# Optimization experiments

Hardware: AMD Instinct MI355X
Metric: run time of the kernel (lower is better)

## Reference

```python
import jax, jax.numpy as jnp
import numpy as np


def _maxpool2x2(x):
    # x: [B, C, H, W] -> [B, C, H//2, W//2]
    B, C, H, W = x.shape
    return x.reshape(B, C, H // 2, 2, W // 2, 2).max(axis=(3, 5))


def setup_inputs() -> dict:
    key = jax.random.key(0)
    ks = jax.random.split(key, 6)
    B, C, H, W = 16, 64, 64, 64
    x = jax.random.normal(ks[0], (B, C, H, W), dtype=jnp.float32)
    w_theta = jax.random.normal(ks[1], (C // 8, C), dtype=jnp.float32) * (1.0 / np.sqrt(C))
    w_phi = jax.random.normal(ks[2], (C // 8, C), dtype=jnp.float32) * (1.0 / np.sqrt(C))
    w_g = jax.random.normal(ks[3], (C // 2, C), dtype=jnp.float32) * (1.0 / np.sqrt(C))
    w_o = jax.random.normal(ks[4], (C, C // 2), dtype=jnp.float32) * (1.0 / np.sqrt(C // 2))
    gamma = jax.random.normal(ks[5], (), dtype=jnp.float32)
    return {"x": x, "w_theta": w_theta, "w_phi": w_phi, "w_g": w_g, "w_o": w_o, "gamma": gamma}


def reference(x, w_theta, w_phi, w_g, w_o, gamma):
    B, C, H, W = x.shape
    S = H * W  # full spatial size
    # 1x1 convs == channel matmuls
    theta = jnp.einsum('oc,bchw->bohw', w_theta, x)            # [B, C/8, H, W]
    phi = _maxpool2x2(jnp.einsum('oc,bchw->bohw', w_phi, x))   # [B, C/8, H/2, W/2]
    g = _maxpool2x2(jnp.einsum('oc,bchw->bohw', w_g, x))       # [B, C/2, H/2, W/2]
    theta_f = theta.reshape(B, C // 8, S)                      # [B, C/8, S]
    phi_f = phi.reshape(B, C // 8, S // 4)                     # [B, C/8, S/4]
    g_f = g.reshape(B, C // 2, S // 4)                         # [B, C/2, S/4]
    # beta = softmax(theta^T @ phi) over key dim
    scores = jnp.einsum('bcs,bct->bst', theta_f, phi_f)        # [B, S, S/4]
    beta = jax.nn.softmax(scores, axis=-1)
    attn = jnp.einsum('bct,bst->bcs', g_f, beta)               # [B, C/2, S]
    o = jnp.einsum('oc,bcs->bos', w_o, attn).reshape(B, C, H, W)
    return gamma * o + x
```

## Files before the change

### kernel.cpp

```cpp
#include <hip/hip_runtime.h>

#define B 16
#define C 64
#define SS 4096
#define TT 1024
#define CQ 8
#define CG 32

typedef _Float16 h4 __attribute__((ext_vector_type(4)));
typedef float f32x16 __attribute__((ext_vector_type(16)));

#if __has_builtin(__builtin_amdgcn_exp2f)
#define EXP2(x) __builtin_amdgcn_exp2f(x)
#else
#define EXP2(x) exp2f(x)
#endif

#define MFMA328(a, b, c) __builtin_amdgcn_mfma_f32_32x32x8f16((a), (b), (c), 0, 0, 0)

__global__ __launch_bounds__(256) void k_proj(
        const float* __restrict__ x, const float* __restrict__ w_theta,
        const float* __restrict__ w_phi, const float* __restrict__ w_g,
        _Float16* __restrict__ theta_t, _Float16* __restrict__ phi_t,
        _Float16* __restrict__ g_blk) {
    int tid = threadIdx.x;
    int W = blockIdx.x * 4 + (tid >> 6);
    int l = tid & 63;
    int ln = l & 31, hi = l >> 5;
    int b = W >> 6, ws = W & 63;
    int rp = ws >> 1, wt = ws & 1;
    int sA = rp * 128 + wt * 32 + ln;

    const float LOG2E = 1.44269504088896f;
    float wsc = 1.f;
    const float* wr0;
    if (ln < 8)       { wr0 = w_theta + ln * C; wsc = LOG2E; }
    else if (ln < 16) { wr0 = w_phi + (ln - 8) * C; }
    else              { wr0 = w_g + (ln - 16) * C; }
    const float* wr1 = w_g + (16 + (ln & 15)) * C;
    bool t1v = ln < 16;

    h4 wa0[8], wa1[8];
#pragma unroll
    for (int kk = 0; kk < 8; ++kk) {
        float4 v0 = *(const float4*)&wr0[8 * kk + 4 * hi];
        float4 v1 = *(const float4*)&wr1[8 * kk + 4 * hi];
        wa0[kk][0] = (_Float16)(v0.x * wsc);
        wa0[kk][1] = (_Float16)(v0.y * wsc);
        wa0[kk][2] = (_Float16)(v0.z * wsc);
        wa0[kk][3] = (_Float16)(v0.w * wsc);
        wa1[kk][0] = t1v ? (_Float16)v1.x : (_Float16)0.f;
        wa1[kk][1] = t1v ? (_Float16)v1.y : (_Float16)0.f;
        wa1[kk][2] = t1v ? (_Float16)v1.z : (_Float16)0.f;
        wa1[kk][3] = t1v ? (_Float16)v1.w : (_Float16)0.f;
    }

    const float* xb = x + ((size_t)b << 18);
    float xA[8][4], xB[8][4];
#pragma unroll
    for (int kk = 0; kk < 8; ++kk)
#pragma unroll
        for (int i = 0; i < 4; ++i) {
            int c = 8 * kk + 4 * hi + i;
            xA[kk][i] = xb[((size_t)c << 12) + sA];
            xB[kk][i] = xb[((size_t)c << 12) + sA + 64];
        }

    f32x16 aA0, aA1, aB0, aB1;
#pragma unroll
    for (int r = 0; r < 16; ++r) { aA0[r] = 0.f; aA1[r] = 0.f; aB0[r] = 0.f; aB1[r] = 0.f; }

#pragma unroll
    for (int kk = 0; kk < 8; ++kk) {
        h4 bA, bB;
#pragma unroll
        for (int i = 0; i < 4; ++i) {
            bA[i] = (_Float16)xA[kk][i];
            bB[i] = (_Float16)xB[kk][i];
        }
        aA0 = MFMA328(wa0[kk], bA, aA0);
        aB0 = MFMA328(wa0[kk], bB, aB0);
        aA1 = MFMA328(wa1[kk], bA, aA1);
        aB1 = MFMA328(wa1[kk], bB, aB1);
    }

    {
        h4 tv;
#pragma unroll
        for (int r = 0; r < 4; ++r) tv[r] = (_Float16)aA0[r];
        *(h4*)&theta_t[(size_t)((b << 12) + sA) * 8 + 4 * hi] = tv;
#pragma unroll
        for (int r = 0; r < 4; ++r) tv[r] = (_Float16)aB0[r];
        *(h4*)&theta_t[(size_t)((b << 12) + sA + 64) * 8 + 4 * hi] = tv;
    }

    int t = rp * 32 + wt * 16 + (ln >> 1);
    float pv[4];
#pragma unroll
    for (int j = 0; j < 4; ++j) {
        float m = fmaxf(aA0[4 + j], aB0[4 + j]);
        m = fmaxf(m, __shfl_xor(m, 1));
        pv[j] = m;
    }
    float gv[4][4];
#pragma unroll
    for (int j = 0; j < 4; ++j) {
        float m0 = fmaxf(aA0[8 + j],  aB0[8 + j]);
        float m1 = fmaxf(aA0[12 + j], aB0[12 + j]);
        float m2 = fmaxf(aA1[j],      aB1[j]);
        float m3 = fmaxf(aA1[4 + j],  aB1[4 + j]);
        gv[0][j] = fmaxf(m0, __shfl_xor(m0, 1));
        gv[1][j] = fmaxf(m1, __shfl_xor(m1, 1));
        gv[2][j] = fmaxf(m2, __shfl_xor(m2, 1));
        gv[3][j] = fmaxf(m3, __shfl_xor(m3, 1));
    }
    if ((l & 1) == 0) {
        h4 pj;
#pragma unroll
        for (int j = 0; j < 4; ++j) pj[j] = (_Float16)pv[j];
        *(h4*)&phi_t[(size_t)((b << 10) + t) * 8 + 4 * hi] = pj;
        _Float16* gb = g_blk + ((size_t)(b * 256 + (t >> 2)) * 32) * 4 + (t & 3);
#pragma unroll
        for (int part = 0; part < 4; ++part) {
            int cbase = part * 8 + 4 * hi;
#pragma unroll
            for (int j = 0; j < 4; ++j)
                gb[(size_t)(cbase + j) * 4] = (_Float16)gv[part][j];
        }
    }
}

__global__ __launch_bounds__(512, 4) void k_attn(
        const float* __restrict__ x, const _Float16* __restrict__ theta_t,
        const _Float16* __restrict__ phi_t, const _Float16* __restrict__ g_blk,
        const float* __restrict__ w_o, const float* __restrict__ gamma_p,
        float* __restrict__ out) {
    __shared__ __align__(16) char smem[81920];
    _Float16* g_sh   = (_Float16*)smem;
    _Float16* phi_sh = (_Float16*)(smem + 65536);
    float (*accx)[16][64] = (float (*)[16][64])smem;
    float (*mlx)[2][64]   = (float (*)[2][64])(smem + 32768);

    int tid = threadIdx.x;
    int bid = blockIdx.x;
    int wg = (bid & 7) * 64 + (bid >> 3);
    int b = wg >> 5;
    int s0 = (wg & 31) * 128;
    int w = tid >> 6;
    int l = tid & 63;
    int ln = l & 31, hi = l >> 5;
    int sub = w & 3, half = w >> 2;
    int sw = s0 + sub * 32;
    int h16 = half * 16;

    {
        const float4* srcg = (const float4*)(g_blk + (size_t)b * (256 * 128));
        float4* dstg = (float4*)smem;
#pragma unroll
        for (int i = 0; i < 8; ++i)
            dstg[tid + 512 * i] = srcg[tid + 512 * i];
        const float4* srcp = (const float4*)(phi_t + ((size_t)b << 10) * 8);
        float4* dstp = (float4*)phi_sh;
#pragma unroll
        for (int i = 0; i < 2; ++i)
            dstp[tid + 512 * i] = srcp[tid + 512 * i];
    }

    h4 bth = *(const h4*)&theta_t[(size_t)((b << 12) + sw + ln) * 8 + 4 * hi];

    const _Float16* phib = phi_t + ((size_t)b << 10) * 8;

    f32x16 zero;
#pragma unroll
    for (int r = 0; r < 16; ++r) zero[r] = 0.f;

#define LD_PHI(t_) (*(const h4*)&phib[(size_t)((t_) * 32 + ln) * 8 + 4 * hi])
#define LD_PHI_S(t_) (*(const h4*)&phi_sh[(size_t)((t_) * 32 + ln) * 8 + 4 * hi])
#define LD_G_S(dst, t_)                                                        \
    {                                                                          \
        _Pragma("unroll")                                                      \
        for (int kk = 0; kk < 4; ++kk)                                         \
            dst[kk] = *(const h4*)&g_sh[(size_t)(((t_) * 8 + 2 * kk + hi) * 32 + ln) * 4]; \
    }
#define FMAX16(dst, sc_)                                                       \
    {                                                                          \
        float y0 = fmaxf(sc_[0], sc_[1]),   y1 = fmaxf(sc_[2], sc_[3]);        \
        float y2 = fmaxf(sc_[4], sc_[5]),   y3 = fmaxf(sc_[6], sc_[7]);        \
        float y4 = fmaxf(sc_[8], sc_[9]),   y5 = fmaxf(sc_[10], sc_[11]);      \
        float y6 = fmaxf(sc_[12], sc_[13]), y7 = fmaxf(sc_[14], sc_[15]);      \
        y0 = fmaxf(y0, y1); y2 = fmaxf(y2, y3);                                \
        y4 = fmaxf(y4, y5); y6 = fmaxf(y6, y7);                                \
        y0 = fmaxf(y0, y2); y4 = fmaxf(y4, y6);                                \
        dst = fmaxf(dst, fmaxf(y0, y4));                                       \
    }

    float mx = -1e30f;
    {
        h4 pa = LD_PHI(h16);
        h4 pb = LD_PHI(h16 + 1);
#pragma unroll 2
        for (int tc = 0; tc < 16; tc += 2) {
            h4 pan = LD_PHI(h16 + ((tc + 2) & 15));
            h4 pbn = LD_PHI(h16 + ((tc + 3) & 15));
            f32x16 sa = MFMA328(pa, bth, zero);
            f32x16 sb = MFMA328(pb, bth, zero);
            FMAX16(mx, sa);
            FMAX16(mx, sb);
            pa = pan;
            pb = pbn;
        }
        mx = fmaxf(mx, __shfl_xor(mx, 32));
    }

    f32x16 cneg;
#pragma unroll
    for (int r = 0; r < 16; ++r) cneg[r] = -mx;

    __syncthreads();

    f32x16 accE = zero, accO = zero;
    float lsum = 0.f;

#pragma unroll 2
    for (int tc = 0; tc < 16; ++tc) {
        int t_ = h16 + tc;
        h4 ap = LD_PHI_S(t_);
        h4 ag[4];
        LD_G_S(ag, t_);

        f32x16 sc = MFMA328(ap, bth, cneg);

        h4 bp[4];
        float pa0 = 0.f, pa1 = 0.f;
#pragma unroll
        for (int kk = 0; kk < 4; ++kk)
#pragma unroll
            for (int i = 0; i < 4; ++i) {
                float p = EXP2(sc[4 * kk + i]);
                if (kk < 2) pa0 += p; else pa1 += p;
                bp[kk][i] = (_Float16)p;
            }
        lsum += pa0 + pa1;

        accE = MFMA328(ag[0], bp[0], accE);
        accO = MFMA328(ag[1], bp[1], accO);
        accE = MFMA328(ag[2], bp[2], accE);
        accO = MFMA328(ag[3], bp[3], accO);
    }
    f32x16 acc = accE + accO;
    lsum += __shfl_xor(lsum, 32);

    __syncthreads();

#pragma unroll
    for (int r = 0; r < 16; ++r) accx[w][r][l] = acc[r];
    mlx[w][0][l] = mx;
    mlx[w][1][l] = lsum;
    __syncthreads();

    int p = w ^ 4;
    float m2 = mlx[p][0][l], l2 = mlx[p][1][l];
    float M = fmaxf(mx, m2);
    float f1 = EXP2(mx - M), f2 = EXP2(m2 - M);
    float lt = lsum * f1 + l2 * f2;
    float linv = 1.f / lt;

    h4 bat[4];
#pragma unroll
    for (int kk = 0; kk < 4; ++kk)
#pragma unroll
        for (int i = 0; i < 4; ++i) {
            float a2 = accx[p][4 * kk + i][l];
            bat[kk][i] = (_Float16)((acc[4 * kk + i] * f1 + a2 * f2) * linv);
        }

    float gm = gamma_p[0];
    h4 a3[4];
#pragma unroll
    for (int kk = 0; kk < 4; ++kk) {
        float4 wv = *(const float4*)&w_o[(half * 32 + ln) * CG + 8 * kk + 4 * hi];
        a3[kk][0] = (_Float16)(wv.x * gm);
        a3[kk][1] = (_Float16)(wv.y * gm);
        a3[kk][2] = (_Float16)(wv.z * gm);
        a3[kk][3] = (_Float16)(wv.w * gm);
    }
    f32x16 d = MFMA328(a3[0], bat[0], zero);
    d = MFMA328(a3[1], bat[1], d);
    d = MFMA328(a3[2], bat[2], d);
    d = MFMA328(a3[3], bat[3], d);
#pragma unroll
    for (int r = 0; r < 16; ++r) {
        int ch = half * 32 + (r & 3) + 8 * (r >> 2) + 4 * hi;
        size_t idx = (((size_t)(b * C + ch)) << 12) + sw + ln;
        out[idx] = d[r] + x[idx];
    }
#undef LD_PHI
#undef LD_PHI_S
#undef LD_G_S
#undef FMAX16
}

extern "C" void kernel_launch(void* const* d_in, const int* in_sizes, int n_in,
                              void* d_out, int out_size, void* d_ws, size_t ws_size,
                              hipStream_t stream) {
    const float* x       = (const float*)d_in[0];
    const float* w_theta = (const float*)d_in[1];
    const float* w_phi   = (const float*)d_in[2];
    const float* w_g     = (const float*)d_in[3];
    const float* w_o     = (const float*)d_in[4];
    const float* gamma   = (const float*)d_in[5];
    float* out = (float*)d_out;

    _Float16* ws      = (_Float16*)d_ws;
    _Float16* theta_t = ws;
    _Float16* phi_t   = theta_t + (size_t)B * SS * 8;
    _Float16* g_blk   = phi_t + (size_t)B * TT * 8;

    k_proj<<<256, 256, 0, stream>>>(x, w_theta, w_phi, w_g, theta_t, phi_t, g_blk);
    k_attn<<<512, 512, 0, stream>>>(x, theta_t, phi_t, g_blk, w_o, gamma, out);
}
```

Before: 31.12 us.

## Switch attention kernel to 16x16x16 MFMA with 1024-thread blocks of 16-query waves

Rewrites k_attn to use 16x16x16 f16 MFMA tiles instead of 32x32x8. Each wave now handles 16 queries, and the block grows to 16 waves (1024 threads) so it still covers 128 queries, split into two halves over keys. Because K=16 is padded from 8 theta channels, half the lanes feed zero theta (kg>=2), which wastes part of the score MFMA. The exp/softmax work per MFMA is smaller and there are more waves per block, aiming at better latency hiding. The risk is larger register and shared-memory contention at 1024 threads, and score-MFMA efficiency is halved.

```diff
diff --git a/kernel.cpp b/kernel.cpp
--- a/kernel.cpp
+++ b/kernel.cpp
@@ -8,6 +8,7 @@
 #define CG 32
 
 typedef _Float16 h4 __attribute__((ext_vector_type(4)));
+typedef float f32x4 __attribute__((ext_vector_type(4)));
 typedef float f32x16 __attribute__((ext_vector_type(16)));
 
 #if __has_builtin(__builtin_amdgcn_exp2f)
@@ -17,6 +18,7 @@
 #endif
 
 #define MFMA328(a, b, c) __builtin_amdgcn_mfma_f32_32x32x8f16((a), (b), (c), 0, 0, 0)
+#define MFMA16(a, b, c) __builtin_amdgcn_mfma_f32_16x16x16f16((a), (b), (c), 0, 0, 0)
 
 __global__ __launch_bounds__(256) void k_proj(
         const float* __restrict__ x, const float* __restrict__ w_theta,
@@ -130,7 +132,7 @@
     }
 }
 
-__global__ __launch_bounds__(512, 4) void k_attn(
+__global__ __launch_bounds__(1024, 8) void k_attn(
         const float* __restrict__ x, const _Float16* __restrict__ theta_t,
         const _Float16* __restrict__ phi_t, const _Float16* __restrict__ g_blk,
         const float* __restrict__ w_o, const float* __restrict__ gamma_p,
@@ -138,8 +140,8 @@
     __shared__ __align__(16) char smem[81920];
     _Float16* g_sh   = (_Float16*)smem;
     _Float16* phi_sh = (_Float16*)(smem + 65536);
-    float (*accx)[16][64] = (float (*)[16][64])smem;
-    float (*mlx)[2][64]   = (float (*)[2][64])(smem + 32768);
+    float (*accx)[8][64] = (float (*)[8][64])smem;
+    float (*mlx)[2][64]  = (float (*)[2][64])(smem + 32768);
 
     int tid = threadIdx.x;
     int bid = blockIdx.x;
@@ -148,156 +150,123 @@
     int s0 = (wg & 31) * 128;
     int w = tid >> 6;
     int l = tid & 63;
-    int ln = l & 31, hi = l >> 5;
-    int sub = w & 3, half = w >> 2;
-    int sw = s0 + sub * 32;
-    int h16 = half * 16;
+    int ln4 = l & 15, kg = l >> 4;
+    int ssub = w & 7, half = w >> 3;
+    int sw = s0 + ssub * 16;
+    int hc = half * 32;
+    int off = (kg & 1) * 4;
 
     {
         const float4* srcg = (const float4*)(g_blk + (size_t)b * (256 * 128));
         float4* dstg = (float4*)smem;
 #pragma unroll
-        for (int i = 0; i < 8; ++i)
-            dstg[tid + 512 * i] = srcg[tid + 512 * i];
+        for (int i = 0; i < 4; ++i)
+            dstg[tid + 1024 * i] = srcg[tid + 1024 * i];
         const float4* srcp = (const float4*)(phi_t + ((size_t)b << 10) * 8);
-        float4* dstp = (float4*)phi_sh;
-#pragma unroll
-        for (int i = 0; i < 2; ++i)
-            dstp[tid + 512 * i] = srcp[tid + 512 * i];
-    }
-
-    h4 bth = *(const h4*)&theta_t[(size_t)((b << 12) + sw + ln) * 8 + 4 * hi];
+        ((float4*)phi_sh)[tid] = srcp[tid];
+    }
+
+    h4 bth = {};
+    if (kg < 2)
+        bth = *(const h4*)&theta_t[(size_t)((b << 12) + sw + ln4) * 8 + 4 * kg];
 
     const _Float16* phib = phi_t + ((size_t)b << 10) * 8;
-
-    f32x16 zero;
-#pragma unroll
-    for (int r = 0; r < 16; ++r) zero[r] = 0.f;
-
-#define LD_PHI(t_) (*(const h4*)&phib[(size_t)((t_) * 32 + ln) * 8 + 4 * hi])
-#define LD_PHI_S(t_) (*(const h4*)&phi_sh[(size_t)((t_) * 32 + ln) * 8 + 4 * hi])
-#define LD_G_S(dst, t_)                                                        \
-    {                                                                          \
-        _Pragma("unroll")                                                      \
-        for (int kk = 0; kk < 4; ++kk)                                         \
-            dst[kk] = *(const h4*)&g_sh[(size_t)(((t_) * 8 + 2 * kk + hi) * 32 + ln) * 4]; \
-    }
-#define FMAX16(dst, sc_)                                                       \
-    {                                                                          \
-        float y0 = fmaxf(sc_[0], sc_[1]),   y1 = fmaxf(sc_[2], sc_[3]);        \
-        float y2 = fmaxf(sc_[4], sc_[5]),   y3 = fmaxf(sc_[6], sc_[7]);        \
-        float y4 = fmaxf(sc_[8], sc_[9]),   y5 = fmaxf(sc_[10], sc_[11]);      \
-        float y6 = fmaxf(sc_[12], sc_[13]), y7 = fmaxf(sc_[14], sc_[15]);      \
-        y0 = fmaxf(y0, y1); y2 = fmaxf(y2, y3);                                \
-        y4 = fmaxf(y4, y5); y6 = fmaxf(y6, y7);                                \
-        y0 = fmaxf(y0, y2); y4 = fmaxf(y4, y6);                                \
-        dst = fmaxf(dst, fmaxf(y0, y4));                                       \
-    }
+    f32x4 zero4 = {0.f, 0.f, 0.f, 0.f};
 
     float mx = -1e30f;
     {
-        h4 pa = LD_PHI(h16);
-        h4 pb = LD_PHI(h16 + 1);
+        h4 pa = *(const h4*)&phib[(size_t)((hc + 0) * 16 + ln4) * 8 + off];
+        h4 pb = *(const h4*)&phib[(size_t)((hc + 1) * 16 + ln4) * 8 + off];
 #pragma unroll 2
-        for (int tc = 0; tc < 16; tc += 2) {
-            h4 pan = LD_PHI(h16 + ((tc + 2) & 15));
-            h4 pbn = LD_PHI(h16 + ((tc + 3) & 15));
-            f32x16 sa = MFMA328(pa, bth, zero);
-            f32x16 sb = MFMA328(pb, bth, zero);
-            FMAX16(mx, sa);
-            FMAX16(mx, sb);
+        for (int tc = 0; tc < 32; tc += 2) {
+            h4 pan = *(const h4*)&phib[(size_t)((hc + ((tc + 2) & 31)) * 16 + ln4) * 8 + off];
+            h4 pbn = *(const h4*)&phib[(size_t)((hc + ((tc + 3) & 31)) * 16 + ln4) * 8 + off];
+            f32x4 sa = MFMA16(pa, bth, zero4);
+            f32x4 sb = MFMA16(pb, bth, zero4);
+            mx = fmaxf(mx, fmaxf(fmaxf(sa[0], sa[1]), fmaxf(sa[2], sa[3])));
+            mx = fmaxf(mx, fmaxf(fmaxf(sb[0], sb[1]), fmaxf(sb[2], sb[3])));
             pa = pan;
             pb = pbn;
         }
+        mx = fmaxf(mx, __shfl_xor(mx, 16));
         mx = fmaxf(mx, __shfl_xor(mx, 32));
     }
-
-    f32x16 cneg;
-#pragma unroll
-    for (int r = 0; r < 16; ++r) cneg[r] = -mx;
+    f32x4 cneg = {-mx, -mx, -mx, -mx};
 
     __syncthreads();
 
-    f32x16 accE = zero, accO = zero;
+    f32x4 accA = zero4, accB = zero4;
     float lsum = 0.f;
-
 #pragma unroll 2
-    for (int tc = 0; tc < 16; ++tc) {
-        int t_ = h16 + tc;
-        h4 ap = LD_PHI_S(t_);
-        h4 ag[4];
-        LD_G_S(ag, t_);
-
-        f32x16 sc = MFMA328(ap, bth, cneg);
-
-        h4 bp[4];
-        float pa0 = 0.f, pa1 = 0.f;
-#pragma unroll
-        for (int kk = 0; kk < 4; ++kk)
-#pragma unroll
-            for (int i = 0; i < 4; ++i) {
-                float p = EXP2(sc[4 * kk + i]);
-                if (kk < 2) pa0 += p; else pa1 += p;
-                bp[kk][i] = (_Float16)p;
-            }
-        lsum += pa0 + pa1;
-
-        accE = MFMA328(ag[0], bp[0], accE);
-        accO = MFMA328(ag[1], bp[1], accO);
-        accE = MFMA328(ag[2], bp[2], accE);
-        accO = MFMA328(ag[3], bp[3], accO);
-    }
-    f32x16 acc = accE + accO;
+    for (int tc = 0; tc < 32; ++tc) {
+        int ck = hc + tc;
+        h4 ap = *(const h4*)&phi_sh[(size_t)(ck * 16 + ln4) * 8 + off];
+        int j = ck * 4 + kg;
+        h4 ag0 = *(const h4*)&g_sh[(size_t)(j * 32 + ln4) * 4];
+        h4 ag1 = *(const h4*)&g_sh[(size_t)(j * 32 + ln4 + 16) * 4];
+
+        f32x4 sc = MFMA16(ap, bth, cneg);
+
+        float p0 = EXP2(sc[0]), p1 = EXP2(sc[1]);
+        float p2 = EXP2(sc[2]), p3 = EXP2(sc[3]);
+        lsum += (p0 + p1) + (p2 + p3);
+        h4 bp;
+        bp[0] = (_Float16)p0; bp[1] = (_Float16)p1;
+        bp[2] = (_Float16)p2; bp[3] = (_Float16)p3;
+
+        accA = MFMA16(ag0, bp, accA);
+        accB = MFMA16(ag1, bp, accB);
+    }
+    lsum += __shfl_xor(lsum, 16);
     lsum += __shfl_xor(lsum, 32);
 
     __syncthreads();
 
 #pragma unroll
-    for (int r = 0; r < 16; ++r) accx[w][r][l] = acc[r];
+    for (int r = 0; r < 4; ++r) {
+        accx[w][r][l] = accA[r];
+        accx[w][4 + r][l] = accB[r];
+    }
     mlx[w][0][l] = mx;
     mlx[w][1][l] = lsum;
     __syncthreads();
 
-    int p = w ^ 4;
+    int p = w ^ 8;
     float m2 = mlx[p][0][l], l2 = mlx[p][1][l];
     float M = fmaxf(mx, m2);
     float f1 = EXP2(mx - M), f2 = EXP2(m2 - M);
-    float lt = lsum * f1 + l2 * f2;
-    float linv = 1.f / lt;
-
-    h4 bat[4];
-#pragma unroll
-    for (int kk = 0; kk < 4; ++kk)
-#pragma unroll
-        for (int i = 0; i < 4; ++i) {
-            float a2 = accx[p][4 * kk + i][l];
-            bat[kk][i] = (_Float16)((acc[4 * kk + i] * f1 + a2 * f2) * linv);
-        }
+    float linv = 1.f / (lsum * f1 + l2 * f2);
+
+    h4 bat0, bat1;
+#pragma unroll
+    for (int i = 0; i < 4; ++i) {
+        bat0[i] = (_Float16)((accA[i] * f1 + accx[p][i][l] * f2) * linv);
+        bat1[i] = (_Float16)((accB[i] * f1 + accx[p][4 + i][l] * f2) * linv);
+    }
 
     float gm = gamma_p[0];
-    h4 a3[4];
-#pragma unroll
-    for (int kk = 0; kk < 4; ++kk) {
-        float4 wv = *(const float4*)&w_o[(half * 32 + ln) * CG + 8 * kk + 4 * hi];
-        a3[kk][0] = (_Float16)(wv.x * gm);
-        a3[kk][1] = (_Float16)(wv.y * gm);
-        a3[kk][2] = (_Float16)(wv.z * gm);
-        a3[kk][3] = (_Float16)(wv.w * gm);
-    }
-    f32x16 d = MFMA328(a3[0], bat[0], zero);
-    d = MFMA328(a3[1], bat[1], d);
-    d = MFMA328(a3[2], bat[2], d);
-    d = MFMA328(a3[3], bat[3], d);
-#pragma unroll
-    for (int r = 0; r < 16; ++r) {
-        int ch = half * 32 + (r & 3) + 8 * (r >> 2) + 4 * hi;
-        size_t idx = (((size_t)(b * C + ch)) << 12) + sw + ln;
-        out[idx] = d[r] + x[idx];
-    }
-#undef LD_PHI
-#undef LD_PHI_S
-#undef LD_G_S
-#undef FMAX16
+    h4 a3[2][2];
+#pragma unroll
+    for (int m = 0; m < 2; ++m)
+#pragma unroll
+        for (int kt = 0; kt < 2; ++kt) {
+            float4 wv = *(const float4*)&w_o[(half * 32 + m * 16 + ln4) * CG + 4 * kg + 16 * kt];
+            a3[m][kt][0] = (_Float16)(wv.x * gm);
+            a3[m][kt][1] = (_Float16)(wv.y * gm);
+            a3[m][kt][2] = (_Float16)(wv.z * gm);
+            a3[m][kt][3] = (_Float16)(wv.w * gm);
+        }
+#pragma unroll
+    for (int m = 0; m < 2; ++m) {
+        f32x4 d = MFMA16(a3[m][0], bat0, zero4);
+        d = MFMA16(a3[m][1], bat1, d);
+#pragma unroll
+        for (int r = 0; r < 4; ++r) {
+            int ch = half * 32 + m * 16 + 4 * kg + r;
+            size_t idx = (((size_t)(b * C + ch)) << 12) + sw + ln4;
+            out[idx] = d[r] + x[idx];
+        }
+    }
 }
 
 extern "C" void kernel_launch(void* const* d_in, const int* in_sizes, int n_in,
@@ -317,5 +286,5 @@
     _Float16* g_blk   = phi_t + (size_t)B * TT * 8;
 
     k_proj<<<256, 256, 0, stream>>>(x, w_theta, w_phi, w_g, theta_t, phi_t, g_blk);
-    k_attn<<<512, 512, 0, stream>>>(x, theta_t, phi_t, g_blk, w_o, gamma, out);
+    k_attn<<<512, 1024, 0, stream>>>(x, theta_t, phi_t, g_blk, w_o, gamma, out);
 }
```

Result: slower. 38.18 us (+22.7%).
